# Kernel tuning notes

Hardware: AMD Instinct MI355X
Metric: run time of the kernel (lower is better)

Reference implementation:

```python
import jax, jax.numpy as jnp
import numpy as np

MAX_N = 21
COORD = 3
TOTAL_T = 100
K_RANK = 3
POWER_STEPS = 10


def _recon_single(D, Wt, u_noise, x_noise):
    """D, Wt: [N,N]; u_noise: [K_RANK,N]; x_noise: [N,3]. Returns X: [N,3]."""
    N = MAX_N
    # dist_to_gram (classical MDS double-centering)
    D_row = jnp.sum(D, 0, keepdims=True) / N
    D_col = jnp.sum(D, 1, keepdims=True) / N
    D_mean = jnp.sum(D) / (N * N)
    B = -0.5 * (D - D_row - D_col + D_mean)
    # low_rank_approx_power: k=3 deflated power iterations, 10 steps each
    A = B
    us = []
    for i in range(K_RANK):
        u = u_noise[i]
        for _ in range(POWER_STEPS):
            # F.normalize(u, dim=0, p=2, eps=0.001)
            u = u / jnp.maximum(jnp.linalg.norm(u), 1e-3)
            u = A @ u
        eig_sq = jnp.sum(u * u)
        u = u / jnp.power(eig_sq + 0.01, 0.25)
        us.append(u)
        A = A - jnp.outer(u, u)
    X0 = jnp.stack(us, -1) + x_noise  # [N,3]

    T = jnp.float32(TOTAL_T)

    def energy(X):
        diff = X[None, :, :] - X[:, None, :]          # [N,N,3], D_X[i,j]=||X_j-X_i||^2
        D_X = jnp.sum(diff * diff, -1) + 0.01
        return jnp.sum(Wt * jnp.square(D - D_X))

    def step(X, t):
        g = jax.grad(energy)(X)
        dX = -0.1 * g
        speed = jnp.sqrt(jnp.sum(dX * dX, 1, keepdims=True) + 1e-3)
        alpha_t = 0.1 + (5.0 - 0.1) * ((T - t) / T)
        scale = alpha_t * jnp.tanh(speed / alpha_t) / speed
        return X + dX * scale, None

    X, _ = jax.lax.scan(step, X0, jnp.arange(TOTAL_T, dtype=jnp.float32))
    return X


def _forward(gnn_edge_out, W1, b1, W2, b2, u_noise, x_noise, batch_size):
    h_nf = W1.shape[1]
    # edge_mlp1 (MLP with 1 layer -> Linear + ReLU)
    edge_out = jax.nn.relu(gnn_edge_out @ W1 + b1)                     # [B*N*N, h]
    emb = jnp.sum(edge_out.reshape(batch_size, MAX_N, MAX_N, h_nf), axis=(1, 2))  # [B, h]
    # edge_mlp2 -> symmetrize -> softplus
    e2 = (edge_out @ W2 + b2).reshape(batch_size, MAX_N, MAX_N, 2)
    e2 = e2 + jnp.transpose(e2, (0, 2, 1, 3))
    dw = jax.nn.softplus(e2)
    D_init = dw[..., 0] * (1.0 - jnp.eye(MAX_N, dtype=dw.dtype))       # [B,N,N]
    W = dw[..., 1]                                                     # [B,N,N]
    X_pred = jax.vmap(_recon_single)(D_init, W, u_noise, x_noise)      # [B,N,3]
    return D_init, W, emb, X_pred


def setup_inputs() -> dict:
    key = jax.random.key(0)
    ks = jax.random.split(key, 5)
    B, h_nf = 1024, 256
    n_edges = B * MAX_N * MAX_N
    return {
        "gnn_edge_out": jax.random.normal(ks[0], (n_edges, h_nf), jnp.float32),
        "W1": jax.random.normal(ks[1], (h_nf, h_nf), jnp.float32) * (1.0 / np.sqrt(h_nf)),
        "b1": jnp.zeros((h_nf,), jnp.float32),
        "W2": jax.random.normal(ks[2], (h_nf, 2), jnp.float32) * (1.0 / np.sqrt(h_nf)),
        "b2": jnp.zeros((2,), jnp.float32),
        "u_noise": jax.random.normal(ks[3], (B, K_RANK, MAX_N), jnp.float32),
        "x_noise": jax.random.normal(ks[4], (B, MAX_N, COORD), jnp.float32),
        "batch_size": B,
    }


def reference(gnn_edge_out, W1, b1, W2, b2, u_noise, x_noise, batch_size):
    return _forward(gnn_edge_out, W1, b1, W2, b2, u_noise, x_noise, batch_size)
```

## Files before the change

### kernel.cpp

```cpp
#include <hip/hip_runtime.h>
#include <hip/hip_bf16.h>
#include <math.h>

#define B_SZ 1024
#define NMAX 21
#define NN 441
#define HNF 256
#define TOT_ROWS (B_SZ * NN)
#define TILES_PB 14
#define TROWS 32

typedef short short8 __attribute__((ext_vector_type(8)));
typedef float float4v __attribute__((ext_vector_type(4)));

__device__ __forceinline__ unsigned short f2bf(float x) {
    union { float f; unsigned int u; } v; v.f = x;
    unsigned int r = v.u + 0x7FFFu + ((v.u >> 16) & 1u);
    return (unsigned short)(r >> 16);
}

__device__ __forceinline__ unsigned pk_bf16(float lo, float hi) {
    __hip_bfloat162 h = __float22bfloat162_rn(float2{lo, hi});
    return *reinterpret_cast<unsigned*>(&h);
}

__device__ __forceinline__ float softplus_fast(float x) {
    float e = __builtin_amdgcn_exp2f(-fabsf(x) * 1.44269504088896f);
    float lg = __builtin_amdgcn_logf(1.f + e);
    return fmaxf(x, 0.f) + 0.69314718055995f * lg;
}

__device__ __forceinline__ float tanh_fast(float x) {
    float e = __builtin_amdgcn_exp2f(x * 2.8853900817779268f);
    float q = __builtin_amdgcn_rcpf(e + 1.f);
    return fmaf(-2.f, q, 1.f);
}

__global__ __launch_bounds__(256) void pack_w1(const float* __restrict__ W1,
                                               short* __restrict__ B0p,
                                               float* __restrict__ emb)
{
    int id = blockIdx.x * 256 + threadIdx.x;
    int j = id & 7, l = (id >> 3) & 63, f = (id >> 9) & 15, s = id >> 13;
    int k = s * 32 + ((l >> 4) << 3) + j;
    int c = (f << 4) + (l & 15);
    B0p[id] = (short)f2bf(W1[k * HNF + c]);
    #pragma unroll
    for (int e = 0; e < 4; e++)
        emb[(size_t)e * 65536 + id] = 0.f;
}

__global__ __launch_bounds__(256, 4) void fused_mlp_bf16(
    const float* __restrict__ gnn, const short* __restrict__ B0p,
    const float* __restrict__ b1, const float* __restrict__ W2,
    const float* __restrict__ b2,
    float* __restrict__ Dreg, float* __restrict__ Wreg, float* __restrict__ emb)
{
    __shared__ __align__(16) char ldsbuf[32768];
    float* stage = (float*)ldsbuf;
    short* Abf   = (short*)ldsbuf;
    __shared__ float red0[4][32];
    __shared__ float red1[4][32];

    const int t = threadIdx.x;
    const int w = t >> 6, l = t & 63;
    const int batch = blockIdx.x / TILES_PB;
    const int tile  = blockIdx.x % TILES_PB;
    const long row0 = (long)batch * NN + (long)tile * TROWS;
    const int vr = (tile == TILES_PB - 1) ? (NN - (TILES_PB - 1) * TROWS) : TROWS;

    #pragma unroll
    for (int i = 0; i < 8; i++) {
        int r = (w << 3) + i;
        long ar = row0 + r;
        if (ar >= (long)TOT_ROWS) ar = TOT_ROWS - 1;
        const float* gsrc = gnn + ar * HNF + (l << 2);
        __builtin_amdgcn_global_load_lds(
            (const __attribute__((address_space(1))) unsigned*)gsrc,
            (__attribute__((address_space(3))) unsigned*)(stage + (r << 8)),
            16, 0, 0);
    }

    uint2 pv[8];
    asm volatile("s_waitcnt vmcnt(4)" ::: "memory");
    #pragma unroll
    for (int i = 0; i < 4; i++) {
        float4 f = *(const float4*)(stage + (((w << 3) + i) << 8) + (l << 2));
        pv[i].x = pk_bf16(f.x, f.y);
        pv[i].y = pk_bf16(f.z, f.w);
    }
    asm volatile("s_waitcnt vmcnt(0)" ::: "memory");
    #pragma unroll
    for (int i = 4; i < 8; i++) {
        float4 f = *(const float4*)(stage + (((w << 3) + i) << 8) + (l << 2));
        pv[i].x = pk_bf16(f.x, f.y);
        pv[i].y = pk_bf16(f.z, f.w);
    }
    __syncthreads();

    const int kk_s = l >> 3;
    const int fk_s = (l >> 1) & 3;
    const int jh_s = l & 1;
    #pragma unroll
    for (int i = 0; i < 8; i++) {
        int r = (w << 3) + i;
        int di = (((kk_s << 1) + (r >> 4)) << 6) | (fk_s << 4) | (r & 15);
        *(uint2*)((char*)Abf + (((size_t)(di ^ kk_s)) << 4) + (jh_s << 3)) = pv[i];
    }
    __syncthreads();

    const int frow = l & 15;
    const int fk   = l >> 4;

    float4v acc[2][4];
    #pragma unroll
    for (int m = 0; m < 2; m++)
        #pragma unroll
        for (int n = 0; n < 4; n++)
            acc[m][n] = (float4v){0.f, 0.f, 0.f, 0.f};

    #pragma unroll 2
    for (int kk = 0; kk < 8; ++kk) {
        short8 bf[4], af[2];
        #pragma unroll
        for (int n = 0; n < 4; n++) {
            int nf = (w << 2) + n;
            size_t off = (size_t)((((kk << 4) + nf) << 6) | l) << 3;
            bf[n] = *(const short8*)(B0p + off);
        }
        #pragma unroll
        for (int m = 0; m < 2; m++) {
            int di = ((((kk << 1) + m) << 6) | l) ^ kk;
            af[m] = *(const short8*)(Abf + (size_t)di * 8);
        }
        #pragma unroll
        for (int m = 0; m < 2; m++)
            #pragma unroll
            for (int n = 0; n < 4; n++)
                acc[m][n] = __builtin_amdgcn_mfma_f32_16x16x32_bf16(af[m], bf[n], acc[m][n], 0, 0, 0);
    }

    float w20[4], w21[4], b1v[4];
    #pragma unroll
    for (int n = 0; n < 4; n++) {
        int cc = (((w << 2) + n) << 4) + frow;
        b1v[n] = b1[cc];
        w20[n] = W2[2 * cc];
        w21[n] = W2[2 * cc + 1];
    }
    float ps0[2][4], ps1[2][4], embp[4] = {0.f, 0.f, 0.f, 0.f};
    #pragma unroll
    for (int m = 0; m < 2; m++)
        #pragma unroll
        for (int j = 0; j < 4; j++) { ps0[m][j] = 0.f; ps1[m][j] = 0.f; }

    #pragma unroll
    for (int m = 0; m < 2; m++)
        #pragma unroll
        for (int n = 0; n < 4; n++)
            #pragma unroll
            for (int j = 0; j < 4; j++) {
                float h = fmaxf(acc[m][n][j] + b1v[n], 0.f);
                ps0[m][j] += h * w20[n];
                ps1[m][j] += h * w21[n];
                int row = (m << 4) + (fk << 2) + j;
                if (row < vr) embp[n] += h;
            }

    #pragma unroll
    for (int off = 1; off < 16; off <<= 1)
        #pragma unroll
        for (int m = 0; m < 2; m++)
            #pragma unroll
            for (int j = 0; j < 4; j++) {
                ps0[m][j] += __shfl_xor(ps0[m][j], off);
                ps1[m][j] += __shfl_xor(ps1[m][j], off);
            }
    if (frow == 0) {
        #pragma unroll
        for (int m = 0; m < 2; m++)
            #pragma unroll
            for (int j = 0; j < 4; j++) {
                int row = (m << 4) + (fk << 2) + j;
                red0[w][row] = ps0[m][j];
                red1[w][row] = ps1[m][j];
            }
    }

    #pragma unroll
    for (int n = 0; n < 4; n++) {
        embp[n] += __shfl_xor(embp[n], 16);
        embp[n] += __shfl_xor(embp[n], 32);
    }
    if (l < 16) {
        #pragma unroll
        for (int n = 0; n < 4; n++)
            atomicAdd(emb + (size_t)batch * 256 + (((w << 2) + n) << 4) + l, embp[n]);
    }

    __syncthreads();
    if (t < vr) {
        float v0 = b2[0] + red0[0][t] + red0[1][t] + red0[2][t] + red0[3][t];
        float v1 = b2[1] + red1[0][t] + red1[1][t] + red1[2][t] + red1[3][t];
        Dreg[row0 + t] = v0;
        Wreg[row0 + t] = v1;
    }
}

__global__ __launch_bounds__(64) void symrecon_kernel(
    float* __restrict__ Dreg, float* __restrict__ Wreg,
    const float* __restrict__ un, const float* __restrict__ xn,
    float* __restrict__ Xo)
{
    const int b = blockIdx.x, l = threadIdx.x;
    __shared__ float R0[NN], R1[NN];
    __shared__ float Rs[22], Us[22], Xs[3][22];

    float* Db = Dreg + (size_t)b * NN;
    float* Wb = Wreg + (size_t)b * NN;
    for (int idx = l; idx < NN; idx += 64) { R0[idx] = Db[idx]; R1[idx] = Wb[idx]; }
    if (l == 0) { Rs[21] = 0.f; Us[21] = 0.f; Xs[0][21] = 0.f; Xs[1][21] = 0.f; Xs[2][21] = 0.f; }
    __syncthreads();

    const int half = l >> 5;
    const int li   = l & 31;
    const bool act = li < NMAX;
    const int li0  = act ? li : 0;
    const int q0   = half * 11;

    float Drow[11], Wrow[11], WD[11];
    float rsh = 0.f;
    #pragma unroll
    for (int j = 0; j < 11; j++) {
        int q = q0 + j;
        bool v = act && (q < NMAX);
        int qc = v ? q : 0;
        float rd = R0[li0 * NMAX + qc] + R0[qc * NMAX + li0];
        float rw = R1[li0 * NMAX + qc] + R1[qc * NMAX + li0];
        float d  = (v && q != li) ? softplus_fast(rd) : 0.f;
        float wv = v ? softplus_fast(rw) : 0.f;
        Drow[j] = d; Wrow[j] = wv; WD[j] = wv * d;
        rsh += d;
    }
    if (act) {
        #pragma unroll
        for (int j = 0; j < 11; j++) {
            int q = q0 + j;
            if (q < NMAX) {
                Db[li * NMAX + q] = Drow[j];
                Wb[li * NMAX + q] = Wrow[j];
            }
        }
    }

    float rsf = rsh + __shfl_xor(rsh, 32);
    float tot = rsh;
    #pragma unroll
    for (int m = 1; m < 64; m <<= 1) tot += __shfl_xor(tot, m);
    const float mean = tot * (1.f / (float)NN);
    const float rsn  = rsf * (1.f / (float)NMAX);
    if (act && half == 0) Rs[li] = rsn;
    float Arow[11];
    #pragma unroll
    for (int j = 0; j < 11; j++) {
        int q = q0 + j;
        bool v = act && (q < NMAX);
        float rsq = Rs[q];
        Arow[j] = v ? -0.5f * (Drow[j] - rsn - rsq + mean) : 0.f;
    }

    float xc[3];
    #pragma unroll
    for (int e = 0; e < 3; e++) {
        float u = act ? un[(size_t)b * 63 + e * NMAX + li] : 0.f;
        for (int s = 0; s < 10; s++) {
            float n2 = (act && half == 0) ? u * u : 0.f;
            #pragma unroll
            for (int m = 1; m < 64; m <<= 1) n2 += __shfl_xor(n2, m);
            u *= fminf(__builtin_amdgcn_rsqf(n2), 1000.f);
            if (act && half == 0) Us[li] = u;
            float a = 0.f;
            #pragma unroll
            for (int j = 0; j < 11; j++) a = fmaf(Arow[j], Us[q0 + j], a);
            a += __shfl_xor(a, 32);
            u = act ? a : 0.f;
        }
        float e2 = (act && half == 0) ? u * u : 0.f;
        #pragma unroll
        for (int m = 1; m < 64; m <<= 1) e2 += __shfl_xor(e2, m);
        u *= sqrtf(__builtin_amdgcn_rsqf(e2 + 0.01f));
        xc[e] = u;
        if (act && half == 0) Us[li] = u;
        #pragma unroll
        for (int j = 0; j < 11; j++) Arow[j] = fmaf(-u, Us[q0 + j], Arow[j]);
    }
    float x = xc[0], y = xc[1], z = xc[2];
    if (act) {
        x += xn[(size_t)b * 63 + li * 3 + 0];
        y += xn[(size_t)b * 63 + li * 3 + 1];
        z += xn[(size_t)b * 63 + li * 3 + 2];
    }
    if (act && half == 0) { Xs[0][li] = x; Xs[1][li] = y; Xs[2][li] = z; }

    for (int tstep = 0; tstep < 100; tstep++) {
        float gx = 0.f, gy = 0.f, gz = 0.f;
        #pragma unroll
        for (int j = 0; j < 11; j++) {
            int q = q0 + j;
            float dx = x - Xs[0][q];
            float dy = y - Xs[1][q];
            float dz = z - Xs[2][q];
            float s  = fmaf(dx, dx, fmaf(dy, dy, fmaf(dz, dz, 0.01f)));
            float cm = fmaf(-Wrow[j], s, WD[j]);
            gx = fmaf(cm, dx, gx);
            gy = fmaf(cm, dy, gy);
            gz = fmaf(cm, dz, gz);
        }
        gx += __shfl_xor(gx, 32);
        gy += __shfl_xor(gy, 32);
        gz += __shfl_xor(gz, 32);
        float d0 = 0.8f * gx, d1 = 0.8f * gy, d2 = 0.8f * gz;
        float ss = fmaf(d0, d0, fmaf(d1, d1, fmaf(d2, d2, 1e-3f)));
        float inv_sp = __builtin_amdgcn_rsqf(ss);
        float speed  = ss * inv_sp;
        float alpha  = fmaf(-0.049f, (float)tstep, 5.0f);
        float th     = tanh_fast(speed * __builtin_amdgcn_rcpf(alpha));
        float scale  = alpha * th * inv_sp;
        x = fmaf(d0, scale, x);
        y = fmaf(d1, scale, y);
        z = fmaf(d2, scale, z);
        if (act && half == 0) { Xs[0][li] = x; Xs[1][li] = y; Xs[2][li] = z; }
    }
    if (act && half == 0) {
        Xo[(size_t)b * 63 + li * 3 + 0] = x;
        Xo[(size_t)b * 63 + li * 3 + 1] = y;
        Xo[(size_t)b * 63 + li * 3 + 2] = z;
    }
}

extern "C" void kernel_launch(void* const* d_in, const int* in_sizes, int n_in,
                              void* d_out, int out_size, void* d_ws, size_t ws_size,
                              hipStream_t stream) {
    const float* gnn = (const float*)d_in[0];
    const float* W1  = (const float*)d_in[1];
    const float* b1  = (const float*)d_in[2];
    const float* W2  = (const float*)d_in[3];
    const float* b2  = (const float*)d_in[4];
    const float* un  = (const float*)d_in[5];
    const float* xn  = (const float*)d_in[6];

    float* out  = (float*)d_out;
    float* Dreg = out;
    float* Wreg = out + (size_t)TOT_ROWS;
    float* emb  = out + (size_t)2 * TOT_ROWS;
    float* Xo   = out + (size_t)2 * TOT_ROWS + B_SZ*256;

    short* B0p = (short*)d_ws;

    pack_w1<<<dim3(256), dim3(256), 0, stream>>>(W1, B0p, emb);

    fused_mlp_bf16<<<dim3(B_SZ * TILES_PB), dim3(256), 0, stream>>>(
        gnn, B0p, b1, W2, b2, Dreg, Wreg, emb);

    symrecon_kernel<<<dim3(B_SZ), dim3(64), 0, stream>>>(Dreg, Wreg, un, xn, Xo);
}
```

Baseline: 245.7 us.

## Make MLP blocks loop over seven tiles with double-buffered LDS prefetch

```diff
diff --git a/kernel.cpp b/kernel.cpp
--- a/kernel.cpp
+++ b/kernel.cpp
@@ -9,6 +9,7 @@
 #define TOT_ROWS (B_SZ * NN)
 #define TILES_PB 14
 #define TROWS 32
+#define TPB 7
 
 typedef short short8 __attribute__((ext_vector_type(8)));
 typedef float float4v __attribute__((ext_vector_type(4)));
@@ -50,95 +51,27 @@
         emb[(size_t)e * 65536 + id] = 0.f;
 }
 
-__global__ __launch_bounds__(256, 4) void fused_mlp_bf16(
+__global__ __launch_bounds__(256, 2) void fused_mlp_bf16(
     const float* __restrict__ gnn, const short* __restrict__ B0p,
     const float* __restrict__ b1, const float* __restrict__ W2,
     const float* __restrict__ b2,
     float* __restrict__ Dreg, float* __restrict__ Wreg, float* __restrict__ emb)
 {
-    __shared__ __align__(16) char ldsbuf[32768];
-    float* stage = (float*)ldsbuf;
-    short* Abf   = (short*)ldsbuf;
+    __shared__ __align__(16) char ldsbuf[2][32768];
     __shared__ float red0[4][32];
     __shared__ float red1[4][32];
 
     const int t = threadIdx.x;
     const int w = t >> 6, l = t & 63;
-    const int batch = blockIdx.x / TILES_PB;
-    const int tile  = blockIdx.x % TILES_PB;
-    const long row0 = (long)batch * NN + (long)tile * TROWS;
-    const int vr = (tile == TILES_PB - 1) ? (NN - (TILES_PB - 1) * TROWS) : TROWS;
-
-    #pragma unroll
-    for (int i = 0; i < 8; i++) {
-        int r = (w << 3) + i;
-        long ar = row0 + r;
-        if (ar >= (long)TOT_ROWS) ar = TOT_ROWS - 1;
-        const float* gsrc = gnn + ar * HNF + (l << 2);
-        __builtin_amdgcn_global_load_lds(
-            (const __attribute__((address_space(1))) unsigned*)gsrc,
-            (__attribute__((address_space(3))) unsigned*)(stage + (r << 8)),
-            16, 0, 0);
-    }
-
-    uint2 pv[8];
-    asm volatile("s_waitcnt vmcnt(4)" ::: "memory");
-    #pragma unroll
-    for (int i = 0; i < 4; i++) {
-        float4 f = *(const float4*)(stage + (((w << 3) + i) << 8) + (l << 2));
-        pv[i].x = pk_bf16(f.x, f.y);
-        pv[i].y = pk_bf16(f.z, f.w);
-    }
-    asm volatile("s_waitcnt vmcnt(0)" ::: "memory");
-    #pragma unroll
-    for (int i = 4; i < 8; i++) {
-        float4 f = *(const float4*)(stage + (((w << 3) + i) << 8) + (l << 2));
-        pv[i].x = pk_bf16(f.x, f.y);
-        pv[i].y = pk_bf16(f.z, f.w);
-    }
-    __syncthreads();
+    const int batch = blockIdx.x >> 1;
+    const int tile0 = (blockIdx.x & 1) * TPB;
+    const long bbase = (long)batch * NN;
 
     const int kk_s = l >> 3;
     const int fk_s = (l >> 1) & 3;
     const int jh_s = l & 1;
-    #pragma unroll
-    for (int i = 0; i < 8; i++) {
-        int r = (w << 3) + i;
-        int di = (((kk_s << 1) + (r >> 4)) << 6) | (fk_s << 4) | (r & 15);
-        *(uint2*)((char*)Abf + (((size_t)(di ^ kk_s)) << 4) + (jh_s << 3)) = pv[i];
-    }
-    __syncthreads();
-
     const int frow = l & 15;
     const int fk   = l >> 4;
-
-    float4v acc[2][4];
-    #pragma unroll
-    for (int m = 0; m < 2; m++)
-        #pragma unroll
-        for (int n = 0; n < 4; n++)
-            acc[m][n] = (float4v){0.f, 0.f, 0.f, 0.f};
-
-    #pragma unroll 2
-    for (int kk = 0; kk < 8; ++kk) {
-        short8 bf[4], af[2];
-        #pragma unroll
-        for (int n = 0; n < 4; n++) {
-            int nf = (w << 2) + n;
-            size_t off = (size_t)((((kk << 4) + nf) << 6) | l) << 3;
-            bf[n] = *(const short8*)(B0p + off);
-        }
-        #pragma unroll
-        for (int m = 0; m < 2; m++) {
-            int di = ((((kk << 1) + m) << 6) | l) ^ kk;
-            af[m] = *(const short8*)(Abf + (size_t)di * 8);
-        }
-        #pragma unroll
-        for (int m = 0; m < 2; m++)
-            #pragma unroll
-            for (int n = 0; n < 4; n++)
-                acc[m][n] = __builtin_amdgcn_mfma_f32_16x16x32_bf16(af[m], bf[n], acc[m][n], 0, 0, 0);
-    }
 
     float w20[4], w21[4], b1v[4];
     #pragma unroll
@@ -148,43 +81,132 @@
         w20[n] = W2[2 * cc];
         w21[n] = W2[2 * cc + 1];
     }
-    float ps0[2][4], ps1[2][4], embp[4] = {0.f, 0.f, 0.f, 0.f};
-    #pragma unroll
-    for (int m = 0; m < 2; m++)
-        #pragma unroll
-        for (int j = 0; j < 4; j++) { ps0[m][j] = 0.f; ps1[m][j] = 0.f; }
-
-    #pragma unroll
-    for (int m = 0; m < 2; m++)
-        #pragma unroll
-        for (int n = 0; n < 4; n++)
-            #pragma unroll
-            for (int j = 0; j < 4; j++) {
-                float h = fmaxf(acc[m][n][j] + b1v[n], 0.f);
-                ps0[m][j] += h * w20[n];
-                ps1[m][j] += h * w21[n];
-                int row = (m << 4) + (fk << 2) + j;
-                if (row < vr) embp[n] += h;
+    const float b20 = b2[0], b21 = b2[1];
+
+    auto DMA = [&](int p, int buf) {
+        const long row0 = bbase + (long)(tile0 + p) * TROWS;
+        float* st = (float*)ldsbuf[buf];
+        #pragma unroll
+        for (int i = 0; i < 8; i++) {
+            int r = (w << 3) + i;
+            long ar = row0 + r;
+            if (ar >= (long)TOT_ROWS) ar = TOT_ROWS - 1;
+            const float* gsrc = gnn + ar * HNF + (l << 2);
+            __builtin_amdgcn_global_load_lds(
+                (const __attribute__((address_space(1))) unsigned*)gsrc,
+                (__attribute__((address_space(3))) unsigned*)(st + (r << 8)),
+                16, 0, 0);
+        }
+    };
+
+    DMA(0, 0);
+    DMA(1, 1);
+
+    float embp[4] = {0.f, 0.f, 0.f, 0.f};
+
+    #pragma unroll 1
+    for (int p = 0; p < TPB; ++p) {
+        const int cur = p & 1;
+        float* stage = (float*)ldsbuf[cur];
+        short* Abf   = (short*)ldsbuf[cur];
+        const int tile = tile0 + p;
+        const long row0 = bbase + (long)tile * TROWS;
+        const int vr = (tile == TILES_PB - 1) ? (NN - (TILES_PB - 1) * TROWS) : TROWS;
+
+        if (p < TPB - 1) asm volatile("s_waitcnt vmcnt(8)" ::: "memory");
+        else             asm volatile("s_waitcnt vmcnt(0)" ::: "memory");
+
+        uint2 pv[8];
+        #pragma unroll
+        for (int i = 0; i < 8; i++) {
+            float4 f = *(const float4*)(stage + (((w << 3) + i) << 8) + (l << 2));
+            pv[i].x = pk_bf16(f.x, f.y);
+            pv[i].y = pk_bf16(f.z, f.w);
+        }
+        __syncthreads();
+        #pragma unroll
+        for (int i = 0; i < 8; i++) {
+            int r = (w << 3) + i;
+            int di = (((kk_s << 1) + (r >> 4)) << 6) | (fk_s << 4) | (r & 15);
+            *(uint2*)((char*)Abf + (((size_t)(di ^ kk_s)) << 4) + (jh_s << 3)) = pv[i];
+        }
+        __syncthreads();
+
+        float4v acc[2][4];
+        #pragma unroll
+        for (int m = 0; m < 2; m++)
+            #pragma unroll
+            for (int n = 0; n < 4; n++)
+                acc[m][n] = (float4v){0.f, 0.f, 0.f, 0.f};
+
+        #pragma unroll 2
+        for (int kk = 0; kk < 8; ++kk) {
+            short8 bf[4], af[2];
+            #pragma unroll
+            for (int n = 0; n < 4; n++) {
+                int nf = (w << 2) + n;
+                size_t off = (size_t)((((kk << 4) + nf) << 6) | l) << 3;
+                bf[n] = *(const short8*)(B0p + off);
             }
-
-    #pragma unroll
-    for (int off = 1; off < 16; off <<= 1)
+            #pragma unroll
+            for (int m = 0; m < 2; m++) {
+                int di = ((((kk << 1) + m) << 6) | l) ^ kk;
+                af[m] = *(const short8*)(Abf + (size_t)di * 8);
+            }
+            #pragma unroll
+            for (int m = 0; m < 2; m++)
+                #pragma unroll
+                for (int n = 0; n < 4; n++)
+                    acc[m][n] = __builtin_amdgcn_mfma_f32_16x16x32_bf16(af[m], bf[n], acc[m][n], 0, 0, 0);
+        }
+
+        float ps0[2][4], ps1[2][4];
         #pragma unroll
         for (int m = 0; m < 2; m++)
             #pragma unroll
-            for (int j = 0; j < 4; j++) {
-                ps0[m][j] += __shfl_xor(ps0[m][j], off);
-                ps1[m][j] += __shfl_xor(ps1[m][j], off);
-            }
-    if (frow == 0) {
+            for (int j = 0; j < 4; j++) { ps0[m][j] = 0.f; ps1[m][j] = 0.f; }
+
         #pragma unroll
         for (int m = 0; m < 2; m++)
             #pragma unroll
-            for (int j = 0; j < 4; j++) {
-                int row = (m << 4) + (fk << 2) + j;
-                red0[w][row] = ps0[m][j];
-                red1[w][row] = ps1[m][j];
-            }
+            for (int n = 0; n < 4; n++)
+                #pragma unroll
+                for (int j = 0; j < 4; j++) {
+                    float h = fmaxf(acc[m][n][j] + b1v[n], 0.f);
+                    ps0[m][j] += h * w20[n];
+                    ps1[m][j] += h * w21[n];
+                    int row = (m << 4) + (fk << 2) + j;
+                    if (row < vr) embp[n] += h;
+                }
+
+        #pragma unroll
+        for (int off = 1; off < 16; off <<= 1)
+            #pragma unroll
+            for (int m = 0; m < 2; m++)
+                #pragma unroll
+                for (int j = 0; j < 4; j++) {
+                    ps0[m][j] += __shfl_xor(ps0[m][j], off);
+                    ps1[m][j] += __shfl_xor(ps1[m][j], off);
+                }
+        if (frow == 0) {
+            #pragma unroll
+            for (int m = 0; m < 2; m++)
+                #pragma unroll
+                for (int j = 0; j < 4; j++) {
+                    int row = (m << 4) + (fk << 2) + j;
+                    red0[w][row] = ps0[m][j];
+                    red1[w][row] = ps1[m][j];
+                }
+        }
+        __syncthreads();
+        if (t < vr) {
+            float v0 = b20 + red0[0][t] + red0[1][t] + red0[2][t] + red0[3][t];
+            float v1 = b21 + red1[0][t] + red1[1][t] + red1[2][t] + red1[3][t];
+            Dreg[row0 + t] = v0;
+            Wreg[row0 + t] = v1;
+        }
+
+        if (p + 2 < TPB) DMA(p + 2, cur);
     }
 
     #pragma unroll
@@ -196,14 +218,6 @@
         #pragma unroll
         for (int n = 0; n < 4; n++)
             atomicAdd(emb + (size_t)batch * 256 + (((w << 2) + n) << 4) + l, embp[n]);
-    }
-
-    __syncthreads();
-    if (t < vr) {
-        float v0 = b2[0] + red0[0][t] + red0[1][t] + red0[2][t] + red0[3][t];
-        float v1 = b2[1] + red1[0][t] + red1[1][t] + red1[2][t] + red1[3][t];
-        Dreg[row0 + t] = v0;
-        Wreg[row0 + t] = v1;
     }
 }
 
@@ -359,7 +373,7 @@
 
     pack_w1<<<dim3(256), dim3(256), 0, stream>>>(W1, B0p, emb);
 
-    fused_mlp_bf16<<<dim3(B_SZ * TILES_PB), dim3(256), 0, stream>>>(
+    fused_mlp_bf16<<<dim3(B_SZ * 2), dim3(256), 0, stream>>>(
         gnn, B0p, b1, W2, b2, Dreg, Wreg, emb);
 
     symrecon_kernel<<<dim3(B_SZ), dim3(64), 0, stream>>>(Dreg, Wreg, un, xn, Xo);
```

Measured after the change: 262.1 us. +6.7%, slower.
